# Performance work log

Measured on AMD Instinct MI355X. Metric: run time of the kernel, lower is better.

The kernel has to match this reference:

```python
import jax, jax.numpy as jnp
import numpy as np

NEG_SLOPE = 0.2  # PyG GATConv default leaky_relu slope


def segment_softmax(logits, seg, num_segments):
    # logits: [E, H], seg: [E] destination node ids
    m = jax.ops.segment_max(logits, seg, num_segments=num_segments)
    m = jnp.where(jnp.isfinite(m), m, 0.0)  # empty segments
    e = jnp.exp(logits - m[seg])
    s = jax.ops.segment_sum(e, seg, num_segments=num_segments)
    return e / (s[seg] + 1e-16)


def gat_conv(x, src, dst, W, att_src, att_dst, bias, heads, out_ch, concat, num_nodes):
    # x: [N, F_in], W: [F_in, heads*out_ch], att_*: [heads, out_ch]
    h = (x @ W).reshape(num_nodes, heads, out_ch)            # [N, H, C]
    a_src = jnp.sum(h * att_src, axis=-1)                    # [N, H]
    a_dst = jnp.sum(h * att_dst, axis=-1)                    # [N, H]
    logits = jax.nn.leaky_relu(a_src[src] + a_dst[dst], NEG_SLOPE)  # [E, H]
    alpha = segment_softmax(logits, dst, num_nodes)          # [E, H]
    msg = h[src] * alpha[..., None]                          # [E, H, C]
    out = jax.ops.segment_sum(msg, dst, num_segments=num_nodes)  # [N, H, C]
    out = out.reshape(num_nodes, heads * out_ch) if concat else out.mean(axis=1)
    return out + bias


def setup_inputs() -> dict:
    key = jax.random.key(0)
    ks = jax.random.split(key, 12)
    N, E = 50000, 800000
    F_in, Hd, H, F_out = 256, 128, 2, 64

    def glorot(k, shape):
        fan = shape[0] + shape[-1]
        return jax.random.normal(k, shape, dtype=jnp.float32) * jnp.sqrt(2.0 / fan)

    x = jax.random.normal(ks[0], (N, F_in), dtype=jnp.float32)
    edge_index = jax.random.randint(ks[1], (2, E), 0, N, dtype=jnp.int32)
    return {
        "x": x,
        "edge_index": edge_index,
        "W1": glorot(ks[2], (F_in, H * Hd)),
        "att_src1": glorot(ks[3], (H, Hd)),
        "att_dst1": glorot(ks[4], (H, Hd)),
        "b1": jnp.zeros((H * Hd,), dtype=jnp.float32),
        "W2": glorot(ks[5], (H * Hd, F_out)),
        "att_src2": glorot(ks[6], (1, F_out)),
        "att_dst2": glorot(ks[7], (1, F_out)),
        "b2": jnp.zeros((F_out,), dtype=jnp.float32),
    }


def reference(x, edge_index, W1, att_src1, att_dst1, b1, W2, att_src2, att_dst2, b2):
    N = x.shape[0]
    # PyG GATConv default: add self loops
    ar = jnp.arange(N, dtype=edge_index.dtype)
    src = jnp.concatenate([edge_index[0], ar])
    dst = jnp.concatenate([edge_index[1], ar])
    # dropout layers are identity in eval mode
    h = gat_conv(x, src, dst, W1, att_src1, att_dst1, b1,
                 heads=2, out_ch=128, concat=True, num_nodes=N)
    h = jax.nn.elu(h)
    out = gat_conv(h, src, dst, W2, att_src2, att_dst2, b2,
                   heads=1, out_ch=64, concat=False, num_nodes=N)
    return jax.nn.log_softmax(out, axis=1)
```

## Files before the change

### kernel.cpp

```cpp
#include <hip/hip_runtime.h>

typedef unsigned short u16;
typedef short bf8_t __attribute__((ext_vector_type(8)));
typedef float f32x4 __attribute__((ext_vector_type(4)));

__device__ inline u16 f2bf(float f) {
  unsigned u = __float_as_uint(f);
  u += 0x7FFFu + ((u >> 16) & 1u);
  return (u16)(u >> 16);
}
__device__ inline float bf2f(u16 h) { return __uint_as_float(((unsigned)h) << 16); }
__device__ inline float bflo(unsigned u) { return __uint_as_float(u << 16); }
__device__ inline float bfhi(unsigned u) { return __uint_as_float(u & 0xffff0000u); }

__global__ void prep_kernel(const int* __restrict__ ei, int E, int N,
                            int* __restrict__ counts,
                            const float* __restrict__ W1, const float* __restrict__ W2,
                            u16* __restrict__ W1T, u16* __restrict__ W2T, int nbc) {
  if ((int)blockIdx.x < nbc) {
    int e = blockIdx.x * 256 + threadIdx.x;
    int Et = E + N;
    if (e < Et) {
      int d = (e < E) ? ei[E + e] : (e - E);
      atomicAdd(&counts[d], 1);
    }
  } else {
    int idx = (blockIdx.x - nbc) * 256 + threadIdx.x;
    if (idx < 256 * 256) {
      int m = idx / 256, k = idx % 256;
      W1T[idx] = f2bf(W1[(size_t)k * 256 + m]);
    } else if (idx < 256 * 256 + 64 * 256) {
      int i = idx - 256 * 256;
      int m = i / 256, k = i % 256;
      W2T[i] = f2bf(W2[(size_t)k * 64 + m]);
    }
  }
}

template<int BM, int BN, int BK, int WM, int WN, bool AF32, int EPI>
__global__ __launch_bounds__(256) void mfma_gemm(const void* __restrict__ Ap,
                                                 const u16* __restrict__ Bt,
                                                 u16* __restrict__ C,
                                                 const float* __restrict__ att_s,
                                                 const float* __restrict__ att_d,
                                                 float* __restrict__ a_s,
                                                 float* __restrict__ a_d,
                                                 int N, int K) {
  constexpr int PAD = 8;
  __shared__ u16 As[BM][BK + PAD];
  __shared__ u16 Bs[BN][BK + PAD];
  const int tid = threadIdx.x;
  const int row0 = blockIdx.x * BM;
  const int w = tid >> 6, lane = tid & 63;
  const int wr = (w / (BN / WN)) * WM;
  const int wc = (w % (BN / WN)) * WN;
  constexpr int MF = WM / 16, NF = WN / 16;
  constexpr int CPR = BK / 8;
  f32x4 acc[MF][NF] = {};

  for (int k0 = 0; k0 < K; k0 += BK) {
    constexpr int ACH = BM * CPR;
#pragma unroll
    for (int c = 0; c < ACH; c += 256) {
      int cc = c + tid;
      int r = cc / CPR, kc = cc % CPR;
      int row = row0 + r;
      if (AF32) {
        const float* A = (const float*)Ap;
        float4 v0 = make_float4(0.f, 0.f, 0.f, 0.f), v1 = v0;
        if (row < N) {
          const float* p = A + (size_t)row * K + k0 + kc * 8;
          v0 = *(const float4*)p;
          v1 = *(const float4*)(p + 4);
        }
        u16 tmp[8] = {f2bf(v0.x), f2bf(v0.y), f2bf(v0.z), f2bf(v0.w),
                      f2bf(v1.x), f2bf(v1.y), f2bf(v1.z), f2bf(v1.w)};
        *(uint4*)&As[r][kc * 8] = *(uint4*)tmp;
      } else {
        const u16* A = (const u16*)Ap;
        uint4 v = make_uint4(0, 0, 0, 0);
        if (row < N) v = *(const uint4*)(A + (size_t)row * K + k0 + kc * 8);
        *(uint4*)&As[r][kc * 8] = v;
      }
    }
    constexpr int BCH = BN * CPR;
#pragma unroll
    for (int c = 0; c < BCH; c += 256) {
      int cc = c + tid;
      int r = cc / CPR, kc = cc % CPR;
      *(uint4*)&Bs[r][kc * 8] = *(const uint4*)(Bt + (size_t)r * K + k0 + kc * 8);
    }
    __syncthreads();
    const int lr = lane & 15, lk = (lane >> 4) * 8;
    bf8_t a[MF], b[NF];
#pragma unroll
    for (int mi = 0; mi < MF; ++mi) a[mi] = *(bf8_t*)&As[wr + mi * 16 + lr][lk];
#pragma unroll
    for (int ni = 0; ni < NF; ++ni) b[ni] = *(bf8_t*)&Bs[wc + ni * 16 + lr][lk];
#pragma unroll
    for (int mi = 0; mi < MF; ++mi)
#pragma unroll
      for (int ni = 0; ni < NF; ++ni)
        acc[mi][ni] = __builtin_amdgcn_mfma_f32_16x16x32_bf16(a[mi], b[ni], acc[mi][ni], 0, 0, 0);
    __syncthreads();
  }
#pragma unroll
  for (int mi = 0; mi < MF; ++mi)
#pragma unroll
    for (int ni = 0; ni < NF; ++ni)
#pragma unroll
      for (int r = 0; r < 4; ++r) {
        int row = row0 + wr + mi * 16 + (lane >> 4) * 4 + r;
        int col = wc + ni * 16 + (lane & 15);
        if (row < N) C[(size_t)row * BN + col] = f2bf(acc[mi][ni][r]);
      }

  if (EPI == 1) {
    __shared__ float sm_s[4][64];
    __shared__ float sm_d[4][64];
    float asl[NF], adl[NF];
#pragma unroll
    for (int ni = 0; ni < NF; ++ni) {
      asl[ni] = att_s[wc + ni * 16 + (lane & 15)];
      adl[ni] = att_d[wc + ni * 16 + (lane & 15)];
    }
#pragma unroll
    for (int mi = 0; mi < MF; ++mi)
#pragma unroll
      for (int r = 0; r < 4; ++r) {
        float ps = 0.f, pd = 0.f;
#pragma unroll
        for (int ni = 0; ni < NF; ++ni) {
          float c = acc[mi][ni][r];
          ps += c * asl[ni];
          pd += c * adl[ni];
        }
#pragma unroll
        for (int o = 1; o < 16; o <<= 1) {
          ps += __shfl_xor(ps, o);
          pd += __shfl_xor(pd, o);
        }
        if ((lane & 15) == 0) {
          int row = mi * 16 + (lane >> 4) * 4 + r;
          sm_s[w][row] = ps;
          sm_d[w][row] = pd;
        }
      }
    __syncthreads();
    if (tid < 128) {
      int row = tid & 63, head = tid >> 6;
      int grow = row0 + row;
      if (grow < N) {
        a_s[grow * 2 + head] = sm_s[head * 2 + 0][row] + sm_s[head * 2 + 1][row];
        a_d[grow * 2 + head] = sm_d[head * 2 + 0][row] + sm_d[head * 2 + 1][row];
      }
    }
  } else if (EPI == 2) {
    float asl[NF], adl[NF];
#pragma unroll
    for (int ni = 0; ni < NF; ++ni) {
      asl[ni] = att_s[ni * 16 + (lane & 15)];
      adl[ni] = att_d[ni * 16 + (lane & 15)];
    }
#pragma unroll
    for (int mi = 0; mi < MF; ++mi)
#pragma unroll
      for (int r = 0; r < 4; ++r) {
        float ps = 0.f, pd = 0.f;
#pragma unroll
        for (int ni = 0; ni < NF; ++ni) {
          float c = acc[mi][ni][r];
          ps += c * asl[ni];
          pd += c * adl[ni];
        }
#pragma unroll
        for (int o = 1; o < 16; o <<= 1) {
          ps += __shfl_xor(ps, o);
          pd += __shfl_xor(pd, o);
        }
        int row = row0 + wr + mi * 16 + (lane >> 4) * 4 + r;
        if ((lane & 15) == 0 && row < N) {
          a_s[row] = ps;
          a_d[row] = pd;
        }
      }
  }
}

__global__ void block_scan_kernel(const int* __restrict__ counts, int* __restrict__ offsets,
                                  int* __restrict__ bsums, int N) {
  __shared__ int sm[256];
  int tid = threadIdx.x;
  int gid = blockIdx.x * 256 + tid;
  int v = (gid < N) ? counts[gid] : 0;
  int val = v;
  sm[tid] = val;
  __syncthreads();
  for (int off = 1; off < 256; off <<= 1) {
    int o = (tid >= off) ? sm[tid - off] : 0;
    __syncthreads();
    val += o;
    sm[tid] = val;
    __syncthreads();
  }
  if (gid < N) offsets[gid] = val - v;
  if (tid == 255) bsums[blockIdx.x] = val;
}

__global__ void scan_sums_kernel(int* __restrict__ bsums, int* __restrict__ offsets,
                                 int nb, int N) {
  __shared__ int sm[1024];
  int tid = threadIdx.x;
  int v = (tid < nb) ? bsums[tid] : 0;
  int val = v;
  sm[tid] = val;
  __syncthreads();
  for (int off = 1; off < 1024; off <<= 1) {
    int o = (tid >= off) ? sm[tid - off] : 0;
    __syncthreads();
    val += o;
    sm[tid] = val;
    __syncthreads();
  }
  if (tid < nb) bsums[tid] = val - v;
  if (tid == 1023) offsets[N] = val;
}

__global__ void add_base_kernel(int* __restrict__ offsets, int* __restrict__ cursor,
                                const int* __restrict__ bsums, int N) {
  int gid = blockIdx.x * 256 + threadIdx.x;
  if (gid >= N) return;
  int o = offsets[gid] + bsums[blockIdx.x];
  offsets[gid] = o;
  cursor[gid] = o;
}

__global__ void scatter_kernel(const int* __restrict__ ei, int E, int N,
                               int* __restrict__ cursor, int* __restrict__ csr_src) {
  int e = blockIdx.x * blockDim.x + threadIdx.x;
  int Et = E + N;
  if (e >= Et) return;
  int s, d;
  if (e < E) { s = ei[e]; d = ei[E + e]; }
  else       { s = d = e - E; }
  int pos = atomicAdd(&cursor[d], 1);
  csr_src[pos] = s;
}

__global__ void agg1_kernel(const u16* __restrict__ H1, const int* __restrict__ offsets,
                            const int* __restrict__ csr_src,
                            const float* __restrict__ a_src, const float* __restrict__ a_dst,
                            const float* __restrict__ b1, u16* __restrict__ out, int N) {
  __shared__ int4 meta[4][64];
  int wv = threadIdx.x >> 6;
  int lane = threadIdx.x & 63;
  int node = blockIdx.x * 4 + wv;
  if (node >= N) return;
  int off = offsets[node];
  int deg = offsets[node + 1] - off;
  float ad0 = a_dst[node * 2 + 0];
  float ad1 = a_dst[node * 2 + 1];
  const int half = lane >> 5;
  const int l5 = lane & 31;
  const bool head1 = (l5 >= 16);
  const char* H1c = (const char*)H1;
  const unsigned loff = (unsigned)(l5 * 16);
  float acc[8] = {0.f, 0.f, 0.f, 0.f, 0.f, 0.f, 0.f, 0.f};
  float den = 0.f;
  const int4* mw = meta[wv];

  auto proc = [&](int jj) {
    int4 m = mw[jj];
    float w = head1 ? __int_as_float(m.z) : __int_as_float(m.y);
    uint4 u = *(const uint4*)(H1c + (((unsigned)m.x << 9) + loff));
    den += w;
    acc[0] += w * bflo(u.x); acc[1] += w * bfhi(u.x);
    acc[2] += w * bflo(u.y); acc[3] += w * bfhi(u.y);
    acc[4] += w * bflo(u.z); acc[5] += w * bfhi(u.z);
    acc[6] += w * bflo(u.w); acc[7] += w * bfhi(u.w);
  };

  for (int base = 0; base < deg; base += 64) {
    int i = base + lane;
    if (i < deg) {
      int s = csr_src[off + i];
      float l0 = a_src[s * 2 + 0] + ad0;
      float l1 = a_src[s * 2 + 1] + ad1;
      l0 = l0 > 0.f ? l0 : 0.2f * l0;
      l1 = l1 > 0.f ? l1 : 0.2f * l1;
      meta[wv][lane] = make_int4(s, __float_as_int(__expf(l0)), __float_as_int(__expf(l1)), 0);
    }
    int cnt = min(64, deg - base);
    int j = 0;
    for (; j + 8 <= cnt; j += 8) {
      proc(j + half); proc(j + 2 + half); proc(j + 4 + half); proc(j + 6 + half);
    }
    for (; j + 2 <= cnt; j += 2) proc(j + half);
    if (j < cnt && half == 0) proc(j);
  }
#pragma unroll
  for (int k = 0; k < 8; ++k) acc[k] += __shfl_xor(acc[k], 32);
  den += __shfl_xor(den, 32);

  float inv = 1.f / (den + 1e-16f);
  float4 b01 = *(const float4*)(b1 + l5 * 8);
  float4 b23 = *(const float4*)(b1 + l5 * 8 + 4);
  float bb[8] = {b01.x, b01.y, b01.z, b01.w, b23.x, b23.y, b23.z, b23.w};
  u16 tmp[8];
#pragma unroll
  for (int k = 0; k < 8; ++k) {
    float o = acc[k] * inv + bb[k];
    o = o > 0.f ? o : expm1f(o);
    tmp[k] = f2bf(o);
  }
  if (half == 0) *(uint4*)(out + (size_t)node * 256 + l5 * 8) = *(uint4*)tmp;
}

__global__ void agg2_kernel(const u16* __restrict__ H2, const int* __restrict__ offsets,
                            const int* __restrict__ csr_src,
                            const float* __restrict__ a_src, const float* __restrict__ a_dst,
                            const float* __restrict__ b2, float* __restrict__ out, int N) {
  __shared__ int2 meta[4][64];
  int wv = threadIdx.x >> 6;
  int lane = threadIdx.x & 63;
  int node = blockIdx.x * 4 + wv;
  if (node >= N) return;
  int off = offsets[node];
  int deg = offsets[node + 1] - off;
  float ad = a_dst[node];
  const int grp = lane >> 3;
  const int l3 = lane & 7;
  const char* H2c = (const char*)H2;
  const unsigned loff = (unsigned)(l3 * 16);
  float acc[8] = {0.f, 0.f, 0.f, 0.f, 0.f, 0.f, 0.f, 0.f};
  float den = 0.f;
  const int2* mw = meta[wv];

  auto proc = [&](int jj) {
    int2 m = mw[jj];
    float w = __int_as_float(m.y);
    uint4 u = *(const uint4*)(H2c + (((unsigned)m.x << 7) + loff));
    den += w;
    acc[0] += w * bflo(u.x); acc[1] += w * bfhi(u.x);
    acc[2] += w * bflo(u.y); acc[3] += w * bfhi(u.y);
    acc[4] += w * bflo(u.z); acc[5] += w * bfhi(u.z);
    acc[6] += w * bflo(u.w); acc[7] += w * bfhi(u.w);
  };

  for (int base = 0; base < deg; base += 64) {
    int i = base + lane;
    if (i < deg) {
      int s = csr_src[off + i];
      float l = a_src[s] + ad;
      l = l > 0.f ? l : 0.2f * l;
      meta[wv][lane] = make_int2(s, __float_as_int(__expf(l)));
    }
    int cnt = min(64, deg - base);
    int j = 0;
    for (; j + 16 <= cnt; j += 16) { proc(j + grp); proc(j + 8 + grp); }
    for (; j + 8 <= cnt; j += 8) proc(j + grp);
    int r = cnt - j;
    if (r > 0 && grp < r) proc(j + grp);
  }
#pragma unroll
  for (int k = 0; k < 8; ++k) {
    acc[k] += __shfl_xor(acc[k], 8);
    acc[k] += __shfl_xor(acc[k], 16);
    acc[k] += __shfl_xor(acc[k], 32);
  }
  den += __shfl_xor(den, 8);
  den += __shfl_xor(den, 16);
  den += __shfl_xor(den, 32);

  float inv = 1.f / (den + 1e-16f);
  float4 b01 = *(const float4*)(b2 + l3 * 8);
  float4 b23 = *(const float4*)(b2 + l3 * 8 + 4);
  float bb[8] = {b01.x, b01.y, b01.z, b01.w, b23.x, b23.y, b23.z, b23.w};
  float v[8];
#pragma unroll
  for (int k = 0; k < 8; ++k) v[k] = acc[k] * inv + bb[k];
  float m = v[0];
#pragma unroll
  for (int k = 1; k < 8; ++k) m = fmaxf(m, v[k]);
  m = fmaxf(m, __shfl_xor(m, 1));
  m = fmaxf(m, __shfl_xor(m, 2));
  m = fmaxf(m, __shfl_xor(m, 4));
  float sum = 0.f;
#pragma unroll
  for (int k = 0; k < 8; ++k) sum += __expf(v[k] - m);
  sum += __shfl_xor(sum, 1);
  sum += __shfl_xor(sum, 2);
  sum += __shfl_xor(sum, 4);
  float ls = m + logf(sum);
  if (lane < 8) {
    float4 o0 = make_float4(v[0] - ls, v[1] - ls, v[2] - ls, v[3] - ls);
    float4 o1 = make_float4(v[4] - ls, v[5] - ls, v[6] - ls, v[7] - ls);
    *(float4*)(out + (size_t)node * 64 + l3 * 8) = o0;
    *(float4*)(out + (size_t)node * 64 + l3 * 8 + 4) = o1;
  }
}

extern "C" void kernel_launch(void* const* d_in, const int* in_sizes, int n_in,
                              void* d_out, int out_size, void* d_ws, size_t ws_size,
                              hipStream_t stream) {
  const float* x   = (const float*)d_in[0];
  const int*   ei  = (const int*)d_in[1];
  const float* W1  = (const float*)d_in[2];
  const float* as1 = (const float*)d_in[3];
  const float* ad1 = (const float*)d_in[4];
  const float* b1  = (const float*)d_in[5];
  const float* W2  = (const float*)d_in[6];
  const float* as2 = (const float*)d_in[7];
  const float* ad2 = (const float*)d_in[8];
  const float* b2  = (const float*)d_in[9];
  float* out = (float*)d_out;

  const int N  = in_sizes[0] / 256;
  const int E  = in_sizes[1] / 2;
  const int Et = E + N;
  const int nb = (N + 255) / 256;
  const int nbc = (Et + 255) / 256;
  const int nbt = (256 * 256 + 64 * 256 + 255) / 256;

  char* p = (char*)d_ws;
  auto alloc = [&](size_t bytes) -> char* {
    char* r = p;
    p += (bytes + 255) & ~(size_t)255;
    return r;
  };
  u16* H1b     = (u16*)alloc((size_t)N * 256 * 2);
  u16* h1act   = (u16*)alloc((size_t)N * 256 * 2);
  u16* H2b     = (u16*)alloc((size_t)N * 64 * 2);
  u16* W1T     = (u16*)alloc((size_t)256 * 256 * 2);
  u16* W2T     = (u16*)alloc((size_t)64 * 256 * 2);
  float* a_src1 = (float*)alloc((size_t)N * 2 * 4);
  float* a_dst1 = (float*)alloc((size_t)N * 2 * 4);
  float* a_src2 = (float*)alloc((size_t)N * 4);
  float* a_dst2 = (float*)alloc((size_t)N * 4);
  int* counts   = (int*)alloc((size_t)N * 4);
  int* offsets  = (int*)alloc((size_t)(N + 1) * 4);
  int* cursor   = (int*)alloc((size_t)N * 4);
  int* bsums    = (int*)alloc((size_t)1024 * 4);
  int* csr_src  = (int*)alloc((size_t)Et * 4);

  const int tb = 256;

  hipMemsetAsync(counts, 0, (size_t)N * 4, stream);
  prep_kernel<<<nbc + nbt, tb, 0, stream>>>(ei, E, N, counts, W1, W2, W1T, W2T, nbc);
  block_scan_kernel<<<nb, 256, 0, stream>>>(counts, offsets, bsums, N);
  scan_sums_kernel<<<1, 1024, 0, stream>>>(bsums, offsets, nb, N);
  add_base_kernel<<<nb, 256, 0, stream>>>(offsets, cursor, bsums, N);
  scatter_kernel<<<(Et + tb - 1) / tb, tb, 0, stream>>>(ei, E, N, cursor, csr_src);

  mfma_gemm<64, 256, 32, 64, 64, true, 1><<<(N + 63) / 64, 256, 0, stream>>>(
      x, W1T, H1b, as1, ad1, a_src1, a_dst1, N, 256);
  agg1_kernel<<<(N + 3) / 4, 256, 0, stream>>>(H1b, offsets, csr_src, a_src1, a_dst1, b1,
                                               h1act, N);

  mfma_gemm<128, 64, 32, 32, 64, false, 2><<<(N + 127) / 128, 256, 0, stream>>>(
      h1act, W2T, H2b, as2, ad2, a_src2, a_dst2, N, 256);
  agg2_kernel<<<(N + 3) / 4, 256, 0, stream>>>(H2b, offsets, csr_src, a_src2, a_dst2, b2,
                                               out, N);
}
```

Measured before the change: 233.1 us.

## Deepen GEMM K-tile, use packed bf16 convert, remap agg1 lanes per edge

The GEMM K tile grows from 32 to 64, with an inner loop over 32-wide MFMA steps, so each barrier pair is amortised over twice the work. The fp32-to-bf16 conversion of A uses the packed __float22bfloat162_rn intrinsic. agg1 now has every lane cover 4 channels of one edge instead of splitting edges between two half-waves with 8 channels each. This removes the final cross-half shuffle reduction but issues narrower 8-byte gathers, and each wave walks edges serially. The larger K tile also doubles LDS use per block, which could lower occupancy.

```diff
diff --git a/kernel.cpp b/kernel.cpp
--- a/kernel.cpp
+++ b/kernel.cpp
@@ -1,4 +1,5 @@
 #include <hip/hip_runtime.h>
+#include <hip/hip_bf16.h>
 
 typedef unsigned short u16;
 typedef short bf8_t __attribute__((ext_vector_type(8)));
@@ -73,9 +74,12 @@
           v0 = *(const float4*)p;
           v1 = *(const float4*)(p + 4);
         }
-        u16 tmp[8] = {f2bf(v0.x), f2bf(v0.y), f2bf(v0.z), f2bf(v0.w),
-                      f2bf(v1.x), f2bf(v1.y), f2bf(v1.z), f2bf(v1.w)};
-        *(uint4*)&As[r][kc * 8] = *(uint4*)tmp;
+        union { __hip_bfloat162 h[4]; uint4 u; } cv;
+        cv.h[0] = __float22bfloat162_rn(make_float2(v0.x, v0.y));
+        cv.h[1] = __float22bfloat162_rn(make_float2(v0.z, v0.w));
+        cv.h[2] = __float22bfloat162_rn(make_float2(v1.x, v1.y));
+        cv.h[3] = __float22bfloat162_rn(make_float2(v1.z, v1.w));
+        *(uint4*)&As[r][kc * 8] = cv.u;
       } else {
         const u16* A = (const u16*)Ap;
         uint4 v = make_uint4(0, 0, 0, 0);
@@ -92,16 +96,19 @@
     }
     __syncthreads();
     const int lr = lane & 15, lk = (lane >> 4) * 8;
-    bf8_t a[MF], b[NF];
-#pragma unroll
-    for (int mi = 0; mi < MF; ++mi) a[mi] = *(bf8_t*)&As[wr + mi * 16 + lr][lk];
-#pragma unroll
-    for (int ni = 0; ni < NF; ++ni) b[ni] = *(bf8_t*)&Bs[wc + ni * 16 + lr][lk];
-#pragma unroll
-    for (int mi = 0; mi < MF; ++mi)
-#pragma unroll
-      for (int ni = 0; ni < NF; ++ni)
-        acc[mi][ni] = __builtin_amdgcn_mfma_f32_16x16x32_bf16(a[mi], b[ni], acc[mi][ni], 0, 0, 0);
+#pragma unroll
+    for (int kk = 0; kk < BK; kk += 32) {
+      bf8_t a[MF], b[NF];
+#pragma unroll
+      for (int mi = 0; mi < MF; ++mi) a[mi] = *(bf8_t*)&As[wr + mi * 16 + lr][kk + lk];
+#pragma unroll
+      for (int ni = 0; ni < NF; ++ni) b[ni] = *(bf8_t*)&Bs[wc + ni * 16 + lr][kk + lk];
+#pragma unroll
+      for (int mi = 0; mi < MF; ++mi)
+#pragma unroll
+        for (int ni = 0; ni < NF; ++ni)
+          acc[mi][ni] = __builtin_amdgcn_mfma_f32_16x16x32_bf16(a[mi], b[ni], acc[mi][ni], 0, 0, 0);
+    }
     __syncthreads();
   }
 #pragma unroll
@@ -260,24 +267,21 @@
   int deg = offsets[node + 1] - off;
   float ad0 = a_dst[node * 2 + 0];
   float ad1 = a_dst[node * 2 + 1];
-  const int half = lane >> 5;
-  const int l5 = lane & 31;
-  const bool head1 = (l5 >= 16);
+  bool hi = lane >= 32;
   const char* H1c = (const char*)H1;
-  const unsigned loff = (unsigned)(l5 * 16);
-  float acc[8] = {0.f, 0.f, 0.f, 0.f, 0.f, 0.f, 0.f, 0.f};
+  const unsigned loff = (unsigned)(lane * 8);
+  float4 acc = make_float4(0.f, 0.f, 0.f, 0.f);
   float den = 0.f;
   const int4* mw = meta[wv];
 
-  auto proc = [&](int jj) {
-    int4 m = mw[jj];
-    float w = head1 ? __int_as_float(m.z) : __int_as_float(m.y);
-    uint4 u = *(const uint4*)(H1c + (((unsigned)m.x << 9) + loff));
+  auto proc = [&](int4 m) {
+    float w = hi ? __int_as_float(m.z) : __int_as_float(m.y);
+    uint2 u = *(const uint2*)(H1c + (((unsigned)m.x << 9) + loff));
     den += w;
-    acc[0] += w * bflo(u.x); acc[1] += w * bfhi(u.x);
-    acc[2] += w * bflo(u.y); acc[3] += w * bfhi(u.y);
-    acc[4] += w * bflo(u.z); acc[5] += w * bfhi(u.z);
-    acc[6] += w * bflo(u.w); acc[7] += w * bfhi(u.w);
+    acc.x += w * bflo(u.x);
+    acc.y += w * bfhi(u.x);
+    acc.z += w * bflo(u.y);
+    acc.w += w * bfhi(u.y);
   };
 
   for (int base = 0; base < deg; base += 64) {
@@ -292,28 +296,26 @@
     }
     int cnt = min(64, deg - base);
     int j = 0;
-    for (; j + 8 <= cnt; j += 8) {
-      proc(j + half); proc(j + 2 + half); proc(j + 4 + half); proc(j + 6 + half);
-    }
-    for (; j + 2 <= cnt; j += 2) proc(j + half);
-    if (j < cnt && half == 0) proc(j);
-  }
-#pragma unroll
-  for (int k = 0; k < 8; ++k) acc[k] += __shfl_xor(acc[k], 32);
-  den += __shfl_xor(den, 32);
-
+    for (; j + 4 <= cnt; j += 4) {
+      int4 m0 = mw[j], m1 = mw[j + 1], m2 = mw[j + 2], m3 = mw[j + 3];
+      proc(m0); proc(m1); proc(m2); proc(m3);
+    }
+    for (; j < cnt; ++j) proc(mw[j]);
+  }
   float inv = 1.f / (den + 1e-16f);
-  float4 b01 = *(const float4*)(b1 + l5 * 8);
-  float4 b23 = *(const float4*)(b1 + l5 * 8 + 4);
-  float bb[8] = {b01.x, b01.y, b01.z, b01.w, b23.x, b23.y, b23.z, b23.w};
-  u16 tmp[8];
-#pragma unroll
-  for (int k = 0; k < 8; ++k) {
-    float o = acc[k] * inv + bb[k];
-    o = o > 0.f ? o : expm1f(o);
-    tmp[k] = f2bf(o);
-  }
-  if (half == 0) *(uint4*)(out + (size_t)node * 256 + l5 * 8) = *(uint4*)tmp;
+  float4 bb = *(const float4*)(b1 + lane * 4);
+  float o0 = acc.x * inv + bb.x;
+  float o1 = acc.y * inv + bb.y;
+  float o2 = acc.z * inv + bb.z;
+  float o3 = acc.w * inv + bb.w;
+  o0 = o0 > 0.f ? o0 : expm1f(o0);
+  o1 = o1 > 0.f ? o1 : expm1f(o1);
+  o2 = o2 > 0.f ? o2 : expm1f(o2);
+  o3 = o3 > 0.f ? o3 : expm1f(o3);
+  uint2 ov;
+  ov.x = (unsigned)f2bf(o0) | ((unsigned)f2bf(o1) << 16);
+  ov.y = (unsigned)f2bf(o2) | ((unsigned)f2bf(o3) << 16);
+  *(uint2*)(out + (size_t)node * 256 + lane * 4) = ov;
 }
 
 __global__ void agg2_kernel(const u16* __restrict__ H2, const int* __restrict__ offsets,
@@ -452,12 +454,12 @@
   add_base_kernel<<<nb, 256, 0, stream>>>(offsets, cursor, bsums, N);
   scatter_kernel<<<(Et + tb - 1) / tb, tb, 0, stream>>>(ei, E, N, cursor, csr_src);
 
-  mfma_gemm<64, 256, 32, 64, 64, true, 1><<<(N + 63) / 64, 256, 0, stream>>>(
+  mfma_gemm<64, 256, 64, 64, 64, true, 1><<<(N + 63) / 64, 256, 0, stream>>>(
       x, W1T, H1b, as1, ad1, a_src1, a_dst1, N, 256);
   agg1_kernel<<<(N + 3) / 4, 256, 0, stream>>>(H1b, offsets, csr_src, a_src1, a_dst1, b1,
                                                h1act, N);
 
-  mfma_gemm<128, 64, 32, 32, 64, false, 2><<<(N + 127) / 128, 256, 0, stream>>>(
+  mfma_gemm<128, 64, 64, 32, 64, false, 2><<<(N + 127) / 128, 256, 0, stream>>>(
       h1act, W2T, H2b, as2, ad2, a_src2, a_dst2, N, 256);
   agg2_kernel<<<(N + 3) / 4, 256, 0, stream>>>(H2b, offsets, csr_src, a_src2, a_dst2, b2,
                                                out, N);
```

Result: no change. 234.9 us (+0.7%).
